# Kernel optimization log

Measured on AMD Instinct MI355X. Metric: run time of the kernel, lower is better.

The kernel has to match this reference:

```python
import jax, jax.numpy as jnp
import numpy as np

B, K, N = 8, 4, 131072
DENSITY = 0.3
NEG_PAD = -1000.0
NEG_IDLE = -1.0e8


def setup_inputs() -> dict:
    rng = np.random.default_rng(0)
    mask_s = rng.random((B, K, N)) < DENSITY  # bool, per-slot variable counts
    mask_a = rng.random((B, K, N)) < DENSITY
    ts = int(mask_s.sum())
    ta = int(mask_a.sum())
    key = jax.random.key(0)
    k1, k2, k3, k4 = jax.random.split(key, 4)
    return {
        "rgb": jax.random.normal(k1, (ts, 3), dtype=jnp.float32),
        "logits_surface": jax.random.normal(k2, (ts, 1), dtype=jnp.float32),
        "logits_air": jax.random.normal(k3, (ta, 1), dtype=jnp.float32),
        "idle_states": (jax.random.uniform(k4, (B, K)) < 0.25).astype(jnp.float32),
        "mask_eval_surface": jnp.asarray(mask_s),
        "mask_eval_air": jnp.asarray(mask_a),
    }


def _expand(mask, values):
    # mask: (B,K,N) bool; values: (total, C) packed in row-major (b,k,n) mask order.
    # Returns (B,K,N,C) where masked positions hold their packed value (others garbage,
    # to be overwritten by the caller's jnp.where). Equivalent to the torch B*K scatter loop.
    m = mask.reshape(-1)
    pos = jnp.cumsum(m.astype(jnp.int32)) - 1  # packed index for each masked slot
    pos = jnp.clip(pos, 0, values.shape[0] - 1)
    return jnp.take(values, pos, axis=0).reshape(mask.shape + (values.shape[-1],))


def reference(rgb, logits_surface, logits_air, idle_states,
              mask_eval_surface, mask_eval_air):
    alive = (1.0 - idle_states)[:, :, None, None]  # (B,K,1,1)
    idle = idle_states[:, :, None, None]
    ms = mask_eval_surface[..., None]  # (B,K,N,1)
    ma = mask_eval_air[..., None]

    rgb_out = jnp.where(ms, _expand(mask_eval_surface, rgb) * alive, 0.0)
    logits_surface_out = jnp.where(
        ms, _expand(mask_eval_surface, logits_surface) * alive + idle * NEG_IDLE, NEG_PAD)
    logits_air_out = jnp.where(
        ma, _expand(mask_eval_air, logits_air) * alive + idle * NEG_IDLE, NEG_PAD)
    return rgb_out, logits_surface_out, logits_air_out
```

## Files before the change

kernel.cpp:

```cpp
#include <hip/hip_runtime.h>
#include <stdint.h>

#define NTOT      4194304LL
#define CHUNK     2048
#define NBLK      2048
#define NEG_PAD   (-1000.0f)
#define NEG_IDLE  (-100000000.0f)

typedef unsigned long long u64;
typedef float float4u __attribute__((ext_vector_type(4), aligned(4)));
typedef float float3u __attribute__((ext_vector_type(3), aligned(4)));
typedef float float4a __attribute__((ext_vector_type(4), aligned(16)));

__global__ __launch_bounds__(256, 8) void count_kernel(
    const int* __restrict__ ms, const int* __restrict__ ma,
    unsigned short* __restrict__ cmp, u64* __restrict__ totals)
{
    const int t = threadIdx.x, lane = t & 63, wave = t >> 6;
    const unsigned bid = blockIdx.x;
    const long long base = (long long)bid * CHUNK;

    const int4* ms4 = (const int4*)(ms + base);
    const int4* ma4 = (const int4*)(ma + base);
    int4 s0 = ms4[2 * t], s1 = ms4[2 * t + 1];
    int4 a0 = ma4[2 * t], a1 = ma4[2 * t + 1];
    unsigned sbits = (unsigned)(s0.x != 0)        | ((unsigned)(s0.y != 0) << 1)
                   | ((unsigned)(s0.z != 0) << 2) | ((unsigned)(s0.w != 0) << 3)
                   | ((unsigned)(s1.x != 0) << 4) | ((unsigned)(s1.y != 0) << 5)
                   | ((unsigned)(s1.z != 0) << 6) | ((unsigned)(s1.w != 0) << 7);
    unsigned abits = (unsigned)(a0.x != 0)        | ((unsigned)(a0.y != 0) << 1)
                   | ((unsigned)(a0.z != 0) << 2) | ((unsigned)(a0.w != 0) << 3)
                   | ((unsigned)(a1.x != 0) << 4) | ((unsigned)(a1.y != 0) << 5)
                   | ((unsigned)(a1.z != 0) << 6) | ((unsigned)(a1.w != 0) << 7);

    cmp[bid * 256u + (unsigned)t] = (unsigned short)(sbits | (abits << 8));

    unsigned cnt = __popc(sbits) | (__popc(abits) << 16);
    #pragma unroll
    for (int o = 32; o; o >>= 1) cnt += __shfl_down(cnt, o, 64);
    __shared__ unsigned lds[4];
    if (lane == 0) lds[wave] = cnt;
    __syncthreads();
    if (t == 0) {
        unsigned tot = lds[0] + lds[1] + lds[2] + lds[3];
        totals[bid] = (u64)(tot & 0xffffu) | ((u64)(tot >> 16) << 32);
    }
}

__global__ __launch_bounds__(256, 6) void expand_kernel(
    const float* __restrict__ rgb, const float* __restrict__ lsurf,
    const float* __restrict__ lair, const float* __restrict__ idle,
    const unsigned short* __restrict__ cmp, const u64* __restrict__ totals,
    unsigned rgb_max, unsigned ts_max, unsigned ta_max,
    float* __restrict__ out_rgb, float* __restrict__ out_ls, float* __restrict__ out_la)
{
    __shared__ unsigned wsum[4];
    __shared__ u64 wacc[4];
    __shared__ unsigned packLDS[256];
    __shared__ unsigned prefLDS[256];
    __shared__ float    rgbLDS[3072];

    const int t = threadIdx.x, lane = t & 63, wave = t >> 6;
    const unsigned bid = blockIdx.x;
    const long long base = (long long)bid * CHUNK;

    unsigned pk = cmp[bid * 256u + (unsigned)t];
    u64 acc = 0;
    #pragma unroll
    for (int j = 0; j < 8; ++j) {
        unsigned idx = (unsigned)t * 8u + (unsigned)j;
        acc += (idx < bid) ? totals[idx] : 0ULL;
    }
    const float idle_v = idle[(int)(base >> 17)];

    packLDS[t] = pk;
    unsigned cnt = __popc(pk & 0xffu) | (__popc(pk >> 8) << 16);

    unsigned x = cnt;
    #pragma unroll
    for (int o = 1; o < 64; o <<= 1) {
        unsigned y = __shfl_up(x, o, 64);
        if (lane >= o) x += y;
    }
    if (lane == 63) wsum[wave] = x;
    #pragma unroll
    for (int o = 32; o; o >>= 1) acc += __shfl_down(acc, o, 64);
    if (lane == 0) wacc[wave] = acc;
    __syncthreads();
    unsigned pre = (wave > 0 ? wsum[0] : 0u) + (wave > 1 ? wsum[1] : 0u)
                 + (wave > 2 ? wsum[2] : 0u);
    prefLDS[t] = pre + x - cnt;
    u64 basesum = wacc[0] + wacc[1] + wacc[2] + wacc[3];
    const unsigned excS = (unsigned)(basesum & 0xffffffffULL);
    const unsigned excA = (unsigned)(basesum >> 32);
    __syncthreads();

    const float alive     = 1.0f - idle_v;
    const float idle_term = idle_v * NEG_IDLE;
    const int  sub = t >> 3, b = t & 7;
    const unsigned bm = (1u << b) - 1u;
    const int  hp = t >> 1;
    const unsigned nib = (unsigned)(t & 1) * 4u;
    const unsigned nm  = (1u << nib) - 1u;

    #pragma unroll
    for (int h = 0; h < 2; ++h) {
        #pragma unroll
        for (int r = 0; r < 4; ++r) {
            const int g = h * 4 + r;
            const int p = (g << 5) + sub;
            unsigned w  = packLDS[p];
            unsigned pv = prefLDS[p];
            unsigned rs = excS + (pv & 0xffffu) + __popc(w & bm);
            const int li = r * 768 + 3 * t;
            if ((w >> b) & 1u) {
                unsigned pr = rs < rgb_max ? rs : rgb_max;
                float3u v = *(const float3u*)(rgb + 3LL * pr);
                rgbLDS[li]     = v.x * alive;
                rgbLDS[li + 1] = v.y * alive;
                rgbLDS[li + 2] = v.z * alive;
            } else {
                rgbLDS[li] = 0.f; rgbLDS[li + 1] = 0.f; rgbLDS[li + 2] = 0.f;
            }
        }
        {
            const int p = h * 128 + hp;
            unsigned w  = packLDS[p];
            unsigned pv = prefLDS[p];
            unsigned ws = w & 0xffu, wa = (w >> 8) & 0xffu;
            unsigned r0s = excS + (pv & 0xffffu) + __popc(ws & nm);
            unsigned r0a = excA + (pv >> 16)     + __popc(wa & nm);
            unsigned sb = (ws >> nib) & 0xFu;
            unsigned ab = (wa >> nib) & 0xFu;
            unsigned rbs = r0s < ts_max - 3u ? r0s : ts_max - 3u;
            unsigned rba = r0a < ta_max - 3u ? r0a : ta_max - 3u;
            float4u Ws = *(const float4u*)(lsurf + rbs);
            float4u Wa = *(const float4u*)(lair  + rba);
            float lsv[4], lav[4];
            #pragma unroll
            for (int j = 0; j < 4; ++j) {
                unsigned mj = (1u << j) - 1u;
                unsigned rj = r0s + __popc(sb & mj);
                unsigned cs = (rj < ts_max ? rj : ts_max) - rbs;
                float vs = cs == 0 ? Ws.x : cs == 1 ? Ws.y : cs == 2 ? Ws.z : Ws.w;
                lsv[j] = ((sb >> j) & 1u) ? vs * alive + idle_term : NEG_PAD;
                unsigned rk = r0a + __popc(ab & mj);
                unsigned ca = (rk < ta_max ? rk : ta_max) - rba;
                float va = ca == 0 ? Wa.x : ca == 1 ? Wa.y : ca == 2 ? Wa.z : Wa.w;
                lav[j] = ((ab >> j) & 1u) ? va * alive + idle_term : NEG_PAD;
            }
            const long long eb = base + h * 1024 + 4 * t;
            float4a vls; vls.x = lsv[0]; vls.y = lsv[1]; vls.z = lsv[2]; vls.w = lsv[3];
            float4a vla; vla.x = lav[0]; vla.y = lav[1]; vla.z = lav[2]; vla.w = lav[3];
            *(float4a*)(out_ls + eb) = vls;
            *(float4a*)(out_la + eb) = vla;
        }
        __syncthreads();
        float4a* dst = (float4a*)(out_rgb + 3 * base) + h * 768;
        const float4a* src = (const float4a*)rgbLDS;
        dst[t]       = src[t];
        dst[t + 256] = src[t + 256];
        dst[t + 512] = src[t + 512];
        __syncthreads();
    }
}

extern "C" void kernel_launch(void* const* d_in, const int* in_sizes, int n_in,
                              void* d_out, int out_size, void* d_ws, size_t ws_size,
                              hipStream_t stream)
{
    const float* rgb   = (const float*)d_in[0];
    const float* lsurf = (const float*)d_in[1];
    const float* lair  = (const float*)d_in[2];
    const float* idle  = (const float*)d_in[3];
    const int*   ms    = (const int*)d_in[4];
    const int*   ma    = (const int*)d_in[5];

    unsigned rgb_max = (unsigned)(in_sizes[0] / 3 - 1);
    unsigned ts_max  = (unsigned)(in_sizes[1] - 1);
    unsigned ta_max  = (unsigned)(in_sizes[2] - 1);

    float* out     = (float*)d_out;
    float* out_rgb = out;
    float* out_ls  = out + NTOT * 3;
    float* out_la  = out_ls + NTOT;

    u64* totals = (u64*)d_ws;
    unsigned short* cmp = (unsigned short*)((char*)d_ws + 16384);

    count_kernel<<<NBLK, 256, 0, stream>>>(ms, ma, cmp, totals);
    expand_kernel<<<NBLK, 256, 0, stream>>>(rgb, lsurf, lair, idle, cmp, totals,
                                            rgb_max, ts_max, ta_max,
                                            out_rgb, out_ls, out_la);
}
```

Measured before the change: 148.0 us.

## Fuse count and expand kernels with single-pass tagged cross-block prefix

Merges the mask-counting kernel into the expand kernel. Each block publishes its tagged per-block totals with a release atomic store and spins on the totals of all earlier blocks to form its exclusive prefix. This drops the second read of the packed masks and the intermediate buffer, at the cost of a memset launch and inter-block spin-waiting that assumes earlier blocks are scheduled first. It also switches the mask loads and output stores to nontemporal loads and stores.

```diff
diff --git a/kernel.cpp b/kernel.cpp
--- a/kernel.cpp
+++ b/kernel.cpp
@@ -11,46 +11,16 @@
 typedef float float4u __attribute__((ext_vector_type(4), aligned(4)));
 typedef float float3u __attribute__((ext_vector_type(3), aligned(4)));
 typedef float float4a __attribute__((ext_vector_type(4), aligned(16)));
+typedef int   int4v   __attribute__((ext_vector_type(4), aligned(16)));
 
-__global__ __launch_bounds__(256, 8) void count_kernel(
-    const int* __restrict__ ms, const int* __restrict__ ma,
-    unsigned short* __restrict__ cmp, u64* __restrict__ totals)
-{
-    const int t = threadIdx.x, lane = t & 63, wave = t >> 6;
-    const unsigned bid = blockIdx.x;
-    const long long base = (long long)bid * CHUNK;
+#define TAG       0x4D17ULL
+#define VALMASK   0xFFFFFFFFFFFFULL
 
-    const int4* ms4 = (const int4*)(ms + base);
-    const int4* ma4 = (const int4*)(ma + base);
-    int4 s0 = ms4[2 * t], s1 = ms4[2 * t + 1];
-    int4 a0 = ma4[2 * t], a1 = ma4[2 * t + 1];
-    unsigned sbits = (unsigned)(s0.x != 0)        | ((unsigned)(s0.y != 0) << 1)
-                   | ((unsigned)(s0.z != 0) << 2) | ((unsigned)(s0.w != 0) << 3)
-                   | ((unsigned)(s1.x != 0) << 4) | ((unsigned)(s1.y != 0) << 5)
-                   | ((unsigned)(s1.z != 0) << 6) | ((unsigned)(s1.w != 0) << 7);
-    unsigned abits = (unsigned)(a0.x != 0)        | ((unsigned)(a0.y != 0) << 1)
-                   | ((unsigned)(a0.z != 0) << 2) | ((unsigned)(a0.w != 0) << 3)
-                   | ((unsigned)(a1.x != 0) << 4) | ((unsigned)(a1.y != 0) << 5)
-                   | ((unsigned)(a1.z != 0) << 6) | ((unsigned)(a1.w != 0) << 7);
-
-    cmp[bid * 256u + (unsigned)t] = (unsigned short)(sbits | (abits << 8));
-
-    unsigned cnt = __popc(sbits) | (__popc(abits) << 16);
-    #pragma unroll
-    for (int o = 32; o; o >>= 1) cnt += __shfl_down(cnt, o, 64);
-    __shared__ unsigned lds[4];
-    if (lane == 0) lds[wave] = cnt;
-    __syncthreads();
-    if (t == 0) {
-        unsigned tot = lds[0] + lds[1] + lds[2] + lds[3];
-        totals[bid] = (u64)(tot & 0xffffu) | ((u64)(tot >> 16) << 32);
-    }
-}
-
-__global__ __launch_bounds__(256, 6) void expand_kernel(
+__global__ __launch_bounds__(256, 6) void fused_kernel(
     const float* __restrict__ rgb, const float* __restrict__ lsurf,
     const float* __restrict__ lair, const float* __restrict__ idle,
-    const unsigned short* __restrict__ cmp, const u64* __restrict__ totals,
+    const int* __restrict__ ms, const int* __restrict__ ma,
+    u64* __restrict__ totals,
     unsigned rgb_max, unsigned ts_max, unsigned ta_max,
     float* __restrict__ out_rgb, float* __restrict__ out_ls, float* __restrict__ out_la)
 {
@@ -64,17 +34,25 @@
     const unsigned bid = blockIdx.x;
     const long long base = (long long)bid * CHUNK;
 
-    unsigned pk = cmp[bid * 256u + (unsigned)t];
-    u64 acc = 0;
-    #pragma unroll
-    for (int j = 0; j < 8; ++j) {
-        unsigned idx = (unsigned)t * 8u + (unsigned)j;
-        acc += (idx < bid) ? totals[idx] : 0ULL;
-    }
+    const int4v* ms4 = (const int4v*)(ms + base);
+    const int4v* ma4 = (const int4v*)(ma + base);
+    int4v s0 = __builtin_nontemporal_load(ms4 + 2 * t);
+    int4v s1 = __builtin_nontemporal_load(ms4 + 2 * t + 1);
+    int4v a0 = __builtin_nontemporal_load(ma4 + 2 * t);
+    int4v a1 = __builtin_nontemporal_load(ma4 + 2 * t + 1);
+    unsigned sbits = (unsigned)(s0[0] != 0)        | ((unsigned)(s0[1] != 0) << 1)
+                   | ((unsigned)(s0[2] != 0) << 2) | ((unsigned)(s0[3] != 0) << 3)
+                   | ((unsigned)(s1[0] != 0) << 4) | ((unsigned)(s1[1] != 0) << 5)
+                   | ((unsigned)(s1[2] != 0) << 6) | ((unsigned)(s1[3] != 0) << 7);
+    unsigned abits = (unsigned)(a0[0] != 0)        | ((unsigned)(a0[1] != 0) << 1)
+                   | ((unsigned)(a0[2] != 0) << 2) | ((unsigned)(a0[3] != 0) << 3)
+                   | ((unsigned)(a1[0] != 0) << 4) | ((unsigned)(a1[1] != 0) << 5)
+                   | ((unsigned)(a1[2] != 0) << 6) | ((unsigned)(a1[3] != 0) << 7);
+    unsigned pk = sbits | (abits << 8);
     const float idle_v = idle[(int)(base >> 17)];
 
     packLDS[t] = pk;
-    unsigned cnt = __popc(pk & 0xffu) | (__popc(pk >> 8) << 16);
+    unsigned cnt = __popc(sbits) | (__popc(abits) << 16);
 
     unsigned x = cnt;
     #pragma unroll
@@ -83,17 +61,40 @@
         if (lane >= o) x += y;
     }
     if (lane == 63) wsum[wave] = x;
+    __syncthreads();
+
+    if (t == 0) {
+        unsigned tot = wsum[0] + wsum[1] + wsum[2] + wsum[3];
+        u64 val = (u64)(tot & 0xffffu) | ((u64)(tot >> 16) << 24) | (TAG << 48);
+        __hip_atomic_store(&totals[bid], val, __ATOMIC_RELEASE,
+                           __HIP_MEMORY_SCOPE_AGENT);
+    }
+    unsigned pre = (wave > 0 ? wsum[0] : 0u) + (wave > 1 ? wsum[1] : 0u)
+                 + (wave > 2 ? wsum[2] : 0u);
+    prefLDS[t] = pre + x - cnt;
+
+    unsigned pend = 0;
+    #pragma unroll
+    for (int j = 0; j < 8; ++j)
+        if ((unsigned)t * 8u + (unsigned)j < bid) pend |= 1u << j;
+    u64 acc = 0;
+    for (int spin = 0; pend && spin < (1 << 16); ++spin) {
+        #pragma unroll
+        for (int j = 0; j < 8; ++j) {
+            if ((pend >> j) & 1u) {
+                u64 v = __hip_atomic_load(&totals[(unsigned)t * 8u + (unsigned)j],
+                                          __ATOMIC_RELAXED, __HIP_MEMORY_SCOPE_AGENT);
+                if ((v >> 48) == TAG) { acc += v & VALMASK; pend &= ~(1u << j); }
+            }
+        }
+    }
     #pragma unroll
     for (int o = 32; o; o >>= 1) acc += __shfl_down(acc, o, 64);
     if (lane == 0) wacc[wave] = acc;
     __syncthreads();
-    unsigned pre = (wave > 0 ? wsum[0] : 0u) + (wave > 1 ? wsum[1] : 0u)
-                 + (wave > 2 ? wsum[2] : 0u);
-    prefLDS[t] = pre + x - cnt;
     u64 basesum = wacc[0] + wacc[1] + wacc[2] + wacc[3];
-    const unsigned excS = (unsigned)(basesum & 0xffffffffULL);
-    const unsigned excA = (unsigned)(basesum >> 32);
-    __syncthreads();
+    const unsigned excS = (unsigned)(basesum & 0xFFFFFFULL);
+    const unsigned excA = (unsigned)((basesum >> 24) & 0xFFFFFFULL);
 
     const float alive     = 1.0f - idle_v;
     const float idle_term = idle_v * NEG_IDLE;
@@ -152,15 +153,15 @@
             const long long eb = base + h * 1024 + 4 * t;
             float4a vls; vls.x = lsv[0]; vls.y = lsv[1]; vls.z = lsv[2]; vls.w = lsv[3];
             float4a vla; vla.x = lav[0]; vla.y = lav[1]; vla.z = lav[2]; vla.w = lav[3];
-            *(float4a*)(out_ls + eb) = vls;
-            *(float4a*)(out_la + eb) = vla;
+            __builtin_nontemporal_store(vls, (float4a*)(out_ls + eb));
+            __builtin_nontemporal_store(vla, (float4a*)(out_la + eb));
         }
         __syncthreads();
         float4a* dst = (float4a*)(out_rgb + 3 * base) + h * 768;
         const float4a* src = (const float4a*)rgbLDS;
-        dst[t]       = src[t];
-        dst[t + 256] = src[t + 256];
-        dst[t + 512] = src[t + 512];
+        __builtin_nontemporal_store(src[t],       dst + t);
+        __builtin_nontemporal_store(src[t + 256], dst + t + 256);
+        __builtin_nontemporal_store(src[t + 512], dst + t + 512);
         __syncthreads();
     }
 }
@@ -186,10 +187,8 @@
     float* out_la  = out_ls + NTOT;
 
     u64* totals = (u64*)d_ws;
-    unsigned short* cmp = (unsigned short*)((char*)d_ws + 16384);
-
-    count_kernel<<<NBLK, 256, 0, stream>>>(ms, ma, cmp, totals);
-    expand_kernel<<<NBLK, 256, 0, stream>>>(rgb, lsurf, lair, idle, cmp, totals,
-                                            rgb_max, ts_max, ta_max,
-                                            out_rgb, out_ls, out_la);
+    hipMemsetAsync(totals, 0, NBLK * sizeof(u64), stream);
+    fused_kernel<<<NBLK, 256, 0, stream>>>(rgb, lsurf, lair, idle, ms, ma, totals,
+                                           rgb_max, ts_max, ta_max,
+                                           out_rgb, out_ls, out_la);
 }
```

Measured after the change: 221.6 us. +49.7%, slower.

## Stage packed block values in LDS and use nontemporal loads/stores

Applied to the files above, without the earlier changes.

Each expand block now cooperatively loads its contiguous slice of packed rgb and logits (up to a cap) into shared memory with coalesced reads. The scatter then reads from LDS instead of issuing scattered global gathers. Mask loads and all output stores become nontemporal to avoid cache pollution. The extra LDS lowers the occupancy target from 6 to 5 blocks, and entries beyond the cap fall back to global loads.

```diff
diff --git a/kernel.cpp b/kernel.cpp
--- a/kernel.cpp
+++ b/kernel.cpp
@@ -6,11 +6,13 @@
 #define NBLK      2048
 #define NEG_PAD   (-1000.0f)
 #define NEG_IDLE  (-100000000.0f)
+#define CAPS      832
+#define CAPA      832
 
 typedef unsigned long long u64;
-typedef float float4u __attribute__((ext_vector_type(4), aligned(4)));
 typedef float float3u __attribute__((ext_vector_type(3), aligned(4)));
 typedef float float4a __attribute__((ext_vector_type(4), aligned(16)));
+typedef int   int4v   __attribute__((ext_vector_type(4), aligned(16)));
 
 __global__ __launch_bounds__(256, 8) void count_kernel(
     const int* __restrict__ ms, const int* __restrict__ ma,
@@ -20,18 +22,20 @@
     const unsigned bid = blockIdx.x;
     const long long base = (long long)bid * CHUNK;
 
-    const int4* ms4 = (const int4*)(ms + base);
-    const int4* ma4 = (const int4*)(ma + base);
-    int4 s0 = ms4[2 * t], s1 = ms4[2 * t + 1];
-    int4 a0 = ma4[2 * t], a1 = ma4[2 * t + 1];
-    unsigned sbits = (unsigned)(s0.x != 0)        | ((unsigned)(s0.y != 0) << 1)
-                   | ((unsigned)(s0.z != 0) << 2) | ((unsigned)(s0.w != 0) << 3)
-                   | ((unsigned)(s1.x != 0) << 4) | ((unsigned)(s1.y != 0) << 5)
-                   | ((unsigned)(s1.z != 0) << 6) | ((unsigned)(s1.w != 0) << 7);
-    unsigned abits = (unsigned)(a0.x != 0)        | ((unsigned)(a0.y != 0) << 1)
-                   | ((unsigned)(a0.z != 0) << 2) | ((unsigned)(a0.w != 0) << 3)
-                   | ((unsigned)(a1.x != 0) << 4) | ((unsigned)(a1.y != 0) << 5)
-                   | ((unsigned)(a1.z != 0) << 6) | ((unsigned)(a1.w != 0) << 7);
+    const int4v* ms4 = (const int4v*)(ms + base);
+    const int4v* ma4 = (const int4v*)(ma + base);
+    int4v s0 = __builtin_nontemporal_load(ms4 + 2 * t);
+    int4v s1 = __builtin_nontemporal_load(ms4 + 2 * t + 1);
+    int4v a0 = __builtin_nontemporal_load(ma4 + 2 * t);
+    int4v a1 = __builtin_nontemporal_load(ma4 + 2 * t + 1);
+    unsigned sbits = (unsigned)(s0[0] != 0)        | ((unsigned)(s0[1] != 0) << 1)
+                   | ((unsigned)(s0[2] != 0) << 2) | ((unsigned)(s0[3] != 0) << 3)
+                   | ((unsigned)(s1[0] != 0) << 4) | ((unsigned)(s1[1] != 0) << 5)
+                   | ((unsigned)(s1[2] != 0) << 6) | ((unsigned)(s1[3] != 0) << 7);
+    unsigned abits = (unsigned)(a0[0] != 0)        | ((unsigned)(a0[1] != 0) << 1)
+                   | ((unsigned)(a0[2] != 0) << 2) | ((unsigned)(a0[3] != 0) << 3)
+                   | ((unsigned)(a1[0] != 0) << 4) | ((unsigned)(a1[1] != 0) << 5)
+                   | ((unsigned)(a1[2] != 0) << 6) | ((unsigned)(a1[3] != 0) << 7);
 
     cmp[bid * 256u + (unsigned)t] = (unsigned short)(sbits | (abits << 8));
 
@@ -47,7 +51,7 @@
     }
 }
 
-__global__ __launch_bounds__(256, 6) void expand_kernel(
+__global__ __launch_bounds__(256, 5) void expand_kernel(
     const float* __restrict__ rgb, const float* __restrict__ lsurf,
     const float* __restrict__ lair, const float* __restrict__ idle,
     const unsigned short* __restrict__ cmp, const u64* __restrict__ totals,
@@ -59,6 +63,9 @@
     __shared__ unsigned packLDS[256];
     __shared__ unsigned prefLDS[256];
     __shared__ float    rgbLDS[3072];
+    __shared__ float    rgbSrc[CAPS * 3];
+    __shared__ float    lsS[CAPS];
+    __shared__ float    laS[CAPA];
 
     const int t = threadIdx.x, lane = t & 63, wave = t >> 6;
     const unsigned bid = blockIdx.x;
@@ -93,6 +100,20 @@
     u64 basesum = wacc[0] + wacc[1] + wacc[2] + wacc[3];
     const unsigned excS = (unsigned)(basesum & 0xffffffffULL);
     const unsigned excA = (unsigned)(basesum >> 32);
+    unsigned totPk = wsum[0] + wsum[1] + wsum[2] + wsum[3];
+    const unsigned totS = totPk & 0xffffu;
+    const unsigned totA = totPk >> 16;
+
+    {
+        const unsigned nS = totS < CAPS ? totS : CAPS;
+        const unsigned nA = totA < CAPA ? totA : CAPA;
+        const float* rgbB = rgb + 3LL * excS;
+        const float* lsB  = lsurf + excS;
+        const float* laB  = lair + excA;
+        for (unsigned i = t; i < nS * 3u; i += 256u) rgbSrc[i] = rgbB[i];
+        for (unsigned i = t; i < nS; i += 256u)      lsS[i]   = lsB[i];
+        for (unsigned i = t; i < nA; i += 256u)      laS[i]   = laB[i];
+    }
     __syncthreads();
 
     const float alive     = 1.0f - idle_v;
@@ -111,14 +132,20 @@
             const int p = (g << 5) + sub;
             unsigned w  = packLDS[p];
             unsigned pv = prefLDS[p];
-            unsigned rs = excS + (pv & 0xffffu) + __popc(w & bm);
             const int li = r * 768 + 3 * t;
             if ((w >> b) & 1u) {
-                unsigned pr = rs < rgb_max ? rs : rgb_max;
-                float3u v = *(const float3u*)(rgb + 3LL * pr);
-                rgbLDS[li]     = v.x * alive;
-                rgbLDS[li + 1] = v.y * alive;
-                rgbLDS[li + 2] = v.z * alive;
+                unsigned lr = (pv & 0xffffu) + __popc(w & bm);
+                float vx, vy, vz;
+                if (lr < CAPS) {
+                    vx = rgbSrc[3 * lr]; vy = rgbSrc[3 * lr + 1]; vz = rgbSrc[3 * lr + 2];
+                } else {
+                    unsigned pr = excS + lr; pr = pr < rgb_max ? pr : rgb_max;
+                    float3u v = *(const float3u*)(rgb + 3LL * pr);
+                    vx = v.x; vy = v.y; vz = v.z;
+                }
+                rgbLDS[li]     = vx * alive;
+                rgbLDS[li + 1] = vy * alive;
+                rgbLDS[li + 2] = vz * alive;
             } else {
                 rgbLDS[li] = 0.f; rgbLDS[li + 1] = 0.f; rgbLDS[li + 2] = 0.f;
             }
@@ -128,39 +155,35 @@
             unsigned w  = packLDS[p];
             unsigned pv = prefLDS[p];
             unsigned ws = w & 0xffu, wa = (w >> 8) & 0xffu;
-            unsigned r0s = excS + (pv & 0xffffu) + __popc(ws & nm);
-            unsigned r0a = excA + (pv >> 16)     + __popc(wa & nm);
+            unsigned baseS = (pv & 0xffffu) + __popc(ws & nm);
+            unsigned baseA = (pv >> 16)     + __popc(wa & nm);
             unsigned sb = (ws >> nib) & 0xFu;
             unsigned ab = (wa >> nib) & 0xFu;
-            unsigned rbs = r0s < ts_max - 3u ? r0s : ts_max - 3u;
-            unsigned rba = r0a < ta_max - 3u ? r0a : ta_max - 3u;
-            float4u Ws = *(const float4u*)(lsurf + rbs);
-            float4u Wa = *(const float4u*)(lair  + rba);
             float lsv[4], lav[4];
             #pragma unroll
             for (int j = 0; j < 4; ++j) {
                 unsigned mj = (1u << j) - 1u;
-                unsigned rj = r0s + __popc(sb & mj);
-                unsigned cs = (rj < ts_max ? rj : ts_max) - rbs;
-                float vs = cs == 0 ? Ws.x : cs == 1 ? Ws.y : cs == 2 ? Ws.z : Ws.w;
+                unsigned rs = baseS + __popc(sb & mj);
+                float vs = rs < CAPS ? lsS[rs]
+                         : lsurf[(excS + rs) < ts_max ? (excS + rs) : ts_max];
                 lsv[j] = ((sb >> j) & 1u) ? vs * alive + idle_term : NEG_PAD;
-                unsigned rk = r0a + __popc(ab & mj);
-                unsigned ca = (rk < ta_max ? rk : ta_max) - rba;
-                float va = ca == 0 ? Wa.x : ca == 1 ? Wa.y : ca == 2 ? Wa.z : Wa.w;
+                unsigned ra = baseA + __popc(ab & mj);
+                float va = ra < CAPA ? laS[ra]
+                         : lair[(excA + ra) < ta_max ? (excA + ra) : ta_max];
                 lav[j] = ((ab >> j) & 1u) ? va * alive + idle_term : NEG_PAD;
             }
             const long long eb = base + h * 1024 + 4 * t;
             float4a vls; vls.x = lsv[0]; vls.y = lsv[1]; vls.z = lsv[2]; vls.w = lsv[3];
             float4a vla; vla.x = lav[0]; vla.y = lav[1]; vla.z = lav[2]; vla.w = lav[3];
-            *(float4a*)(out_ls + eb) = vls;
-            *(float4a*)(out_la + eb) = vla;
+            __builtin_nontemporal_store(vls, (float4a*)(out_ls + eb));
+            __builtin_nontemporal_store(vla, (float4a*)(out_la + eb));
         }
         __syncthreads();
         float4a* dst = (float4a*)(out_rgb + 3 * base) + h * 768;
         const float4a* src = (const float4a*)rgbLDS;
-        dst[t]       = src[t];
-        dst[t + 256] = src[t + 256];
-        dst[t + 512] = src[t + 512];
+        __builtin_nontemporal_store(src[t],       dst + t);
+        __builtin_nontemporal_store(src[t + 256], dst + t + 256);
+        __builtin_nontemporal_store(src[t + 512], dst + t + 512);
         __syncthreads();
     }
 }
```

Result: no change. 150.0 us (+1.4%).
